# Kernel tuning notes

Hardware: AMD Instinct MI355X
Metric: run time of the kernel (lower is better)

The kernel has to match this reference:

```python
import jax, jax.numpy as jnp
import numpy as np

N = 8192
F_IN = 256
F_OUT = 128
SLOPE = 0.2
NEG_INF = -9000000000000000.0


def setup_inputs() -> dict:
    key = jax.random.key(0)
    k1, k2, k3, k4, k5 = jax.random.split(key, 5)
    x = jax.random.normal(k1, (N, F_IN), dtype=jnp.float32)
    adj = jax.random.randint(k2, (N, N), 0, 2).astype(jnp.float32)
    W = jax.random.normal(k3, (F_IN, F_OUT), dtype=jnp.float32) * (1.0 / np.sqrt(F_IN))
    a_src = jax.random.normal(k4, (F_OUT,), dtype=jnp.float32) * (1.0 / np.sqrt(F_OUT))
    a_dst = jax.random.normal(k5, (F_OUT,), dtype=jnp.float32) * (1.0 / np.sqrt(F_OUT))
    return {"x": x, "adj": adj, "W": W, "a_src": a_src, "a_dst": a_dst}


def reference(x, adj, W, a_src, a_dst):
    # h: (N, F_OUT)
    h = x @ W
    f_src = h @ a_src  # (N,)
    f_dst = h @ a_dst  # (N,)
    # additive attention scores: (N, N)
    e = f_src[:, None] + f_dst[None, :]
    e = jnp.where(e >= 0, e, SLOPE * e)  # leaky_relu
    e = jnp.where(adj > 0, e, NEG_INF)
    alpha = jax.nn.softmax(e, axis=1)  # (N, N)
    return alpha @ h  # (N, F_OUT)
```

## Files before the change

kernel.cpp:

```cpp
#include <hip/hip_runtime.h>
#include <hip/hip_bf16.h>

#define NN 8192
#define FIN 256
#define FO 128
#define ROWS 32
#define NCH 32
#define L2E 1.4426950408889634f
#define C2  0.28853900817779268f

typedef __bf16 bf16x8 __attribute__((ext_vector_type(8)));
typedef __bf16 bf16x2 __attribute__((ext_vector_type(2)));
typedef float  f32x4  __attribute__((ext_vector_type(4)));
typedef unsigned long long u64;
typedef u64 u64x2 __attribute__((ext_vector_type(2)));

__device__ __forceinline__ f32x4 ntload(const float* p) {
  return __builtin_nontemporal_load((const f32x4*)p);
}

__global__ __launch_bounds__(256) void k_proj(
    const float* __restrict__ x, const float* __restrict__ W,
    const float* __restrict__ a_src, const float* __restrict__ a_dst,
    __bf16* __restrict__ Bp, float* __restrict__ f_src, float* __restrict__ f_dst)
{
  __shared__ float xs[16 * FIN];
  __shared__ float fs[16], fd[16];
  const int tid = threadIdx.x;
  const int i0 = blockIdx.x * 16;

  const float4* xg = (const float4*)(x + (size_t)i0 * FIN);
  float4* xs4 = (float4*)xs;
  #pragma unroll
  for (int t = 0; t < 4; t++) xs4[tid + 256 * t] = xg[tid + 256 * t];
  if (tid < 16) { fs[tid] = 0.f; fd[tid] = 0.f; }
  __syncthreads();

  const int cq = tid & 31;
  const int rg = tid >> 5;
  const int c0 = cq * 4;
  const int r0 = rg * 2;
  float acc0[4] = {0.f,0.f,0.f,0.f};
  float acc1[4] = {0.f,0.f,0.f,0.f};
  const float* xr0 = xs + r0 * FIN;
  const float* xr1 = xs + (r0 + 1) * FIN;

  for (int k = 0; k < FIN; k += 4) {
    float4 xa = *(const float4*)(xr0 + k);
    float4 xb = *(const float4*)(xr1 + k);
    #pragma unroll
    for (int kk = 0; kk < 4; kk++) {
      float4 wv = *(const float4*)(W + (size_t)(k + kk) * FO + c0);
      float xav = ((const float*)&xa)[kk];
      float xbv = ((const float*)&xb)[kk];
      acc0[0] += xav * wv.x; acc0[1] += xav * wv.y;
      acc0[2] += xav * wv.z; acc0[3] += xav * wv.w;
      acc1[0] += xbv * wv.x; acc1[1] += xbv * wv.y;
      acc1[2] += xbv * wv.z; acc1[3] += xbv * wv.w;
    }
  }

  float4 as = *(const float4*)(a_src + c0);
  float4 ad = *(const float4*)(a_dst + c0);
  float ps0 = acc0[0]*as.x + acc0[1]*as.y + acc0[2]*as.z + acc0[3]*as.w;
  float ps1 = acc1[0]*as.x + acc1[1]*as.y + acc1[2]*as.z + acc1[3]*as.w;
  float pd0 = acc0[0]*ad.x + acc0[1]*ad.y + acc0[2]*ad.z + acc0[3]*ad.w;
  float pd1 = acc1[0]*ad.x + acc1[1]*ad.y + acc1[2]*ad.z + acc1[3]*ad.w;
  atomicAdd(&fs[r0],     ps0);
  atomicAdd(&fs[r0 + 1], ps1);
  atomicAdd(&fd[r0],     pd0);
  atomicAdd(&fd[r0 + 1], pd1);

  const int j0 = i0 + r0;
  const int kg = j0 >> 5;
  const int q  = (j0 >> 3) & 3;
  const int t0 = j0 & 7;
  #pragma unroll
  for (int c = 0; c < 4; c++) {
    const int n = c0 + c;
    bf16x2 v;
    v[0] = (__bf16)acc0[c];
    v[1] = (__bf16)acc1[c];
    size_t idx = ((size_t)(kg * 8 + (n >> 4)) * 64 + q * 16 + (n & 15)) * 8 + t0;
    *(bf16x2*)(Bp + idx) = v;
  }
  __syncthreads();
  if (tid < 16) { f_src[i0 + tid] = fs[tid]; f_dst[i0 + tid] = fd[tid]; }
}

__global__ __launch_bounds__(640) void k_attn(
    const float* __restrict__ adj, const __bf16* __restrict__ Bp,
    const float* __restrict__ f_src, const float* __restrict__ f_dst,
    float* __restrict__ out)
{
  __shared__ __align__(16) float G1[NN];
  __shared__ __align__(16) float G2[NN];
  __shared__ __align__(16) u64 msk[2][ROWS][5];
  __shared__ __align__(16) __bf16 af[2][2][8][64][8];
  __shared__ float lsum[ROWS];

  const int tid = threadIdx.x;
  const int w = tid >> 6;
  const int lane = tid & 63;
  const int i0 = blockIdx.x * ROWS;

  if (w >= 8) {
    const int pw = w - 8;
    const int prow0 = pw * 16;
    const float* abase = adj + (size_t)(i0 + prow0) * NN + lane * 4;

    f32x4 s0,s1,s2,s3,s4,s5,s6,s7,s8,s9,s10,s11,s12,s13,s14,s15;

#define PLOAD(c) {                                                            \
    const float* _b = abase + (size_t)(c) * 256;                              \
    s0=ntload(_b);        s1=ntload(_b+NN);       s2=ntload(_b+2*NN);         \
    s3=ntload(_b+3*NN);   s4=ntload(_b+4*NN);     s5=ntload(_b+5*NN);         \
    s6=ntload(_b+6*NN);   s7=ntload(_b+7*NN);     s8=ntload(_b+8*NN);         \
    s9=ntload(_b+9*NN);   s10=ntload(_b+10*NN);   s11=ntload(_b+11*NN);       \
    s12=ntload(_b+12*NN); s13=ntload(_b+13*NN);   s14=ntload(_b+14*NN);       \
    s15=ntload(_b+15*NN); }

#define PROW(sv, slot, r) {                                                   \
    u64 b0=__ballot(sv[0]>0.f), b1=__ballot(sv[1]>0.f);                       \
    u64 b2=__ballot(sv[2]>0.f), b3=__ballot(sv[3]>0.f);                       \
    if (lane < 4)                                                             \
      msk[slot][prow0 + (r)][lane] = lane==0?b0:lane==1?b1:lane==2?b2:b3; }

#define PPACK(slot) {                                                         \
    PROW(s0,slot,0)  PROW(s1,slot,1)  PROW(s2,slot,2)  PROW(s3,slot,3)        \
    PROW(s4,slot,4)  PROW(s5,slot,5)  PROW(s6,slot,6)  PROW(s7,slot,7)        \
    PROW(s8,slot,8)  PROW(s9,slot,9)  PROW(s10,slot,10) PROW(s11,slot,11)     \
    PROW(s12,slot,12) PROW(s13,slot,13) PROW(s14,slot,14) PROW(s15,slot,15) }

    PLOAD(0)
    PPACK(0)
    PLOAD(1)
    asm volatile("s_waitcnt lgkmcnt(0)" ::: "memory");
    __builtin_amdgcn_s_barrier();
    __builtin_amdgcn_sched_barrier(0);

    for (int k = 0; k < NCH; ++k) {
      if (k + 1 < NCH) {
        PPACK((k + 1) & 1)
        if (k + 2 < NCH) PLOAD(k + 2)
      }
      asm volatile("s_waitcnt lgkmcnt(0)" ::: "memory");
      __builtin_amdgcn_s_barrier();
      __builtin_amdgcn_sched_barrier(0);
    }
    __syncthreads();
#undef PLOAD
#undef PROW
#undef PPACK
  } else {
    const int m = lane & 15;
    const int q = lane >> 4;
    const int mt = w >> 2;
    const int ss = w & 3;
    const int nq = w & 3;

    #pragma unroll
    for (int t = 0; t < NN / 512; ++t) {
      int j = t * 512 + tid;
      float d = f_dst[j];
      G1[j] = __builtin_amdgcn_exp2f(d * L2E);
      G2[j] = __builtin_amdgcn_exp2f(d * C2);
    }
    if (tid < ROWS) lsum[tid] = 0.f;
    float s = f_src[i0 + mt * 16 + m];
    const float F1 = __builtin_amdgcn_exp2f(s * L2E);
    const float F2 = __builtin_amdgcn_exp2f(s * C2);

    f32x4 acc0 = (f32x4){0.f, 0.f, 0.f, 0.f};
    f32x4 acc1 = (f32x4){0.f, 0.f, 0.f, 0.f};
    float psum = 0.f;
    const int r0l = mt * 16 + m;

    __syncthreads();

    for (int c = 0; c < NCH; ++c) {
      const int cur = c & 1;

      {
        u64x2 Ma01 = *(const u64x2*)&msk[cur][r0l][0];
        u64x2 Ma23 = *(const u64x2*)&msk[cur][r0l][2];
        const u64 M0 = Ma01[0], M1 = Ma01[1], M2 = Ma23[0], M3 = Ma23[1];
        #pragma unroll
        for (int kg = 0; kg < 2; ++kg) {
          const int jj = c * 256 + ss * 64 + kg * 32 + q * 8;
          float4 u0 = *(const float4*)(G1 + jj);
          float4 u1 = *(const float4*)(G1 + jj + 4);
          float4 v0 = *(const float4*)(G2 + jj);
          float4 v1 = *(const float4*)(G2 + jj + 4);
          const unsigned b = ss * 16 + kg * 8 + q * 2;
          const unsigned e0 = (unsigned)(M0 >> b);
          const unsigned e1 = (unsigned)(M1 >> b);
          const unsigned e2 = (unsigned)(M2 >> b);
          const unsigned e3 = (unsigned)(M3 >> b);
          float p0 = (e0 & 1u) ? fmaxf(F1 * u0.x, F2 * v0.x) : 0.f;
          float p1 = (e1 & 1u) ? fmaxf(F1 * u0.y, F2 * v0.y) : 0.f;
          float p2 = (e2 & 1u) ? fmaxf(F1 * u0.z, F2 * v0.z) : 0.f;
          float p3 = (e3 & 1u) ? fmaxf(F1 * u0.w, F2 * v0.w) : 0.f;
          float p4 = (e0 & 2u) ? fmaxf(F1 * u1.x, F2 * v1.x) : 0.f;
          float p5 = (e1 & 2u) ? fmaxf(F1 * u1.y, F2 * v1.y) : 0.f;
          float p6 = (e2 & 2u) ? fmaxf(F1 * u1.z, F2 * v1.z) : 0.f;
          float p7 = (e3 & 2u) ? fmaxf(F1 * u1.w, F2 * v1.w) : 0.f;
          psum += ((p0 + p1) + (p2 + p3)) + ((p4 + p5) + (p6 + p7));
          bf16x8 a;
          a[0] = (__bf16)p0; a[1] = (__bf16)p1; a[2] = (__bf16)p2;
          a[3] = (__bf16)p3; a[4] = (__bf16)p4; a[5] = (__bf16)p5;
          a[6] = (__bf16)p6; a[7] = (__bf16)p7;
          *(bf16x8*)&af[cur][mt][ss * 2 + kg][lane][0] = a;
        }
      }
      __syncthreads();

      {
        const __bf16* bch = Bp + (size_t)c * 8 * 4096 + (size_t)(nq * 2) * 512 + lane * 8;
        const bf16x8* afp = (const bf16x8*)&af[cur][mt][0][lane][0];
        #pragma unroll
        for (int h = 0; h < 2; ++h) {
          bf16x8 b00 = *(const bf16x8*)(bch + (h * 4 + 0) * 4096);
          bf16x8 b10 = *(const bf16x8*)(bch + (h * 4 + 0) * 4096 + 512);
          bf16x8 b01 = *(const bf16x8*)(bch + (h * 4 + 1) * 4096);
          bf16x8 b11 = *(const bf16x8*)(bch + (h * 4 + 1) * 4096 + 512);
          bf16x8 b02 = *(const bf16x8*)(bch + (h * 4 + 2) * 4096);
          bf16x8 b12 = *(const bf16x8*)(bch + (h * 4 + 2) * 4096 + 512);
          bf16x8 b03 = *(const bf16x8*)(bch + (h * 4 + 3) * 4096);
          bf16x8 b13 = *(const bf16x8*)(bch + (h * 4 + 3) * 4096 + 512);
          bf16x8 a0 = afp[(h * 4 + 0) * 64];
          bf16x8 a1 = afp[(h * 4 + 1) * 64];
          bf16x8 a2 = afp[(h * 4 + 2) * 64];
          bf16x8 a3 = afp[(h * 4 + 3) * 64];
          acc0 = __builtin_amdgcn_mfma_f32_16x16x32_bf16(a0, b00, acc0, 0, 0, 0);
          acc1 = __builtin_amdgcn_mfma_f32_16x16x32_bf16(a0, b10, acc1, 0, 0, 0);
          acc0 = __builtin_amdgcn_mfma_f32_16x16x32_bf16(a1, b01, acc0, 0, 0, 0);
          acc1 = __builtin_amdgcn_mfma_f32_16x16x32_bf16(a1, b11, acc1, 0, 0, 0);
          acc0 = __builtin_amdgcn_mfma_f32_16x16x32_bf16(a2, b02, acc0, 0, 0, 0);
          acc1 = __builtin_amdgcn_mfma_f32_16x16x32_bf16(a2, b12, acc1, 0, 0, 0);
          acc0 = __builtin_amdgcn_mfma_f32_16x16x32_bf16(a3, b03, acc0, 0, 0, 0);
          acc1 = __builtin_amdgcn_mfma_f32_16x16x32_bf16(a3, b13, acc1, 0, 0, 0);
        }
      }
    }

    {
      float p = psum;
      p += __shfl_xor(p, 16);
      p += __shfl_xor(p, 32);
      if (lane < 16) atomicAdd(&lsum[mt * 16 + lane], p);
    }
    __syncthreads();

    const int rr0 = mt * 16 + q * 4;
    #pragma unroll
    for (int r = 0; r < 4; ++r) {
      const float inv = 1.0f / lsum[rr0 + r];
      float* orow = out + (size_t)(i0 + rr0 + r) * FO + (nq * 2) * 16 + m;
      orow[0]  = acc0[r] * inv;
      orow[16] = acc1[r] * inv;
    }
  }
}

extern "C" void kernel_launch(void* const* d_in, const int* in_sizes, int n_in,
                              void* d_out, int out_size, void* d_ws, size_t ws_size,
                              hipStream_t stream) {
  const float* x     = (const float*)d_in[0];
  const float* adj   = (const float*)d_in[1];
  const float* W     = (const float*)d_in[2];
  const float* a_src = (const float*)d_in[3];
  const float* a_dst = (const float*)d_in[4];
  float* out = (float*)d_out;

  char* ws = (char*)d_ws;
  __bf16* Bp   = (__bf16*)ws;
  float* f_src = (float*)(ws + 2097152);
  float* f_dst = (float*)(ws + 2097152 + 32768);

  hipLaunchKernelGGL(k_proj, dim3(512), dim3(256), 0, stream,
                     x, W, a_src, a_dst, Bp, f_src, f_dst);
  hipLaunchKernelGGL(k_attn, dim3(256), dim3(640), 0, stream,
                     adj, Bp, f_src, f_dst, out);
}
```

Before: 402.9 us.

## Move adjacency bitmask packing into the prep kernel across the whole GPU

Before, the attention kernel had two producer waves per block that streamed the fp32 adjacency and packed it into bitmasks in LDS alongside the compute waves. Now a separate set of 2048 blocks in the projection kernel packs all of adj into a global 8 MB bitmask buffer. The attention kernel reads its masks directly from global memory with a one-chunk register prefetch and runs with 512 threads. The goal is to spread the 256 MB adj read across all CUs, since the attention grid has only 256 blocks. The cost is an extra global write and read of the bitmask and a serialization point between the two kernels.

```diff
diff --git a/kernel.cpp b/kernel.cpp
--- a/kernel.cpp
+++ b/kernel.cpp
@@ -15,11 +15,8 @@
 typedef unsigned long long u64;
 typedef u64 u64x2 __attribute__((ext_vector_type(2)));
 
-__device__ __forceinline__ f32x4 ntload(const float* p) {
-  return __builtin_nontemporal_load((const f32x4*)p);
-}
-
-__global__ __launch_bounds__(256) void k_proj(
+__global__ __launch_bounds__(256) void k_prep(
+    const float* __restrict__ adj, u64* __restrict__ ab,
     const float* __restrict__ x, const float* __restrict__ W,
     const float* __restrict__ a_src, const float* __restrict__ a_dst,
     __bf16* __restrict__ Bp, float* __restrict__ f_src, float* __restrict__ f_dst)
@@ -27,7 +24,37 @@
   __shared__ float xs[16 * FIN];
   __shared__ float fs[16], fd[16];
   const int tid = threadIdx.x;
-  const int i0 = blockIdx.x * 16;
+
+  if (blockIdx.x < 2048) {
+    const int w = tid >> 6, lane = tid & 63;
+    const int row = blockIdx.x * 4 + w;
+    const float4* src = (const float4*)(adj + (size_t)row * NN) + lane;
+    u64* dst = ab + (size_t)row * 128;
+
+    for (int g = 0; g < 32; g += 2) {
+      float4 va = src[g * 64];
+      float4 vb = src[g * 64 + 64];
+      u64 a0 = __ballot(va.x > 0.f);
+      u64 a1 = __ballot(va.y > 0.f);
+      u64 a2 = __ballot(va.z > 0.f);
+      u64 a3 = __ballot(va.w > 0.f);
+      if (lane < 4) {
+        u64 mv = lane == 0 ? a0 : lane == 1 ? a1 : lane == 2 ? a2 : a3;
+        dst[g * 4 + lane] = mv;
+      }
+      u64 b0 = __ballot(vb.x > 0.f);
+      u64 b1 = __ballot(vb.y > 0.f);
+      u64 b2 = __ballot(vb.z > 0.f);
+      u64 b3 = __ballot(vb.w > 0.f);
+      if (lane < 4) {
+        u64 mv = lane == 0 ? b0 : lane == 1 ? b1 : lane == 2 ? b2 : b3;
+        dst[(g + 1) * 4 + lane] = mv;
+      }
+    }
+    return;
+  }
+
+  const int i0 = (blockIdx.x - 2048) * 16;
 
   const float4* xg = (const float4*)(x + (size_t)i0 * FIN);
   float4* xs4 = (float4*)xs;
@@ -88,178 +115,133 @@
   if (tid < 16) { f_src[i0 + tid] = fs[tid]; f_dst[i0 + tid] = fd[tid]; }
 }
 
-__global__ __launch_bounds__(640) void k_attn(
-    const float* __restrict__ adj, const __bf16* __restrict__ Bp,
+__global__ __launch_bounds__(512) void k_attn(
+    const u64* __restrict__ ab, const __bf16* __restrict__ Bp,
     const float* __restrict__ f_src, const float* __restrict__ f_dst,
     float* __restrict__ out)
 {
   __shared__ __align__(16) float G1[NN];
   __shared__ __align__(16) float G2[NN];
-  __shared__ __align__(16) u64 msk[2][ROWS][5];
   __shared__ __align__(16) __bf16 af[2][2][8][64][8];
   __shared__ float lsum[ROWS];
 
   const int tid = threadIdx.x;
   const int w = tid >> 6;
   const int lane = tid & 63;
+  const int m = lane & 15;
+  const int q = lane >> 4;
   const int i0 = blockIdx.x * ROWS;
-
-  if (w >= 8) {
-    const int pw = w - 8;
-    const int prow0 = pw * 16;
-    const float* abase = adj + (size_t)(i0 + prow0) * NN + lane * 4;
-
-    f32x4 s0,s1,s2,s3,s4,s5,s6,s7,s8,s9,s10,s11,s12,s13,s14,s15;
-
-#define PLOAD(c) {                                                            \
-    const float* _b = abase + (size_t)(c) * 256;                              \
-    s0=ntload(_b);        s1=ntload(_b+NN);       s2=ntload(_b+2*NN);         \
-    s3=ntload(_b+3*NN);   s4=ntload(_b+4*NN);     s5=ntload(_b+5*NN);         \
-    s6=ntload(_b+6*NN);   s7=ntload(_b+7*NN);     s8=ntload(_b+8*NN);         \
-    s9=ntload(_b+9*NN);   s10=ntload(_b+10*NN);   s11=ntload(_b+11*NN);       \
-    s12=ntload(_b+12*NN); s13=ntload(_b+13*NN);   s14=ntload(_b+14*NN);       \
-    s15=ntload(_b+15*NN); }
-
-#define PROW(sv, slot, r) {                                                   \
-    u64 b0=__ballot(sv[0]>0.f), b1=__ballot(sv[1]>0.f);                       \
-    u64 b2=__ballot(sv[2]>0.f), b3=__ballot(sv[3]>0.f);                       \
-    if (lane < 4)                                                             \
-      msk[slot][prow0 + (r)][lane] = lane==0?b0:lane==1?b1:lane==2?b2:b3; }
-
-#define PPACK(slot) {                                                         \
-    PROW(s0,slot,0)  PROW(s1,slot,1)  PROW(s2,slot,2)  PROW(s3,slot,3)        \
-    PROW(s4,slot,4)  PROW(s5,slot,5)  PROW(s6,slot,6)  PROW(s7,slot,7)        \
-    PROW(s8,slot,8)  PROW(s9,slot,9)  PROW(s10,slot,10) PROW(s11,slot,11)     \
-    PROW(s12,slot,12) PROW(s13,slot,13) PROW(s14,slot,14) PROW(s15,slot,15) }
-
-    PLOAD(0)
-    PPACK(0)
-    PLOAD(1)
-    asm volatile("s_waitcnt lgkmcnt(0)" ::: "memory");
-    __builtin_amdgcn_s_barrier();
-    __builtin_amdgcn_sched_barrier(0);
-
-    for (int k = 0; k < NCH; ++k) {
-      if (k + 1 < NCH) {
-        PPACK((k + 1) & 1)
-        if (k + 2 < NCH) PLOAD(k + 2)
-      }
-      asm volatile("s_waitcnt lgkmcnt(0)" ::: "memory");
-      __builtin_amdgcn_s_barrier();
-      __builtin_amdgcn_sched_barrier(0);
+  const int mt = w >> 2;
+  const int sq = w & 3;
+
+  const u64* mrow = ab + (size_t)(i0 + mt * 16 + m) * 128;
+  u64x2 Mlo = *(const u64x2*)(mrow);
+  u64x2 Mhi = *(const u64x2*)(mrow + 2);
+
+  #pragma unroll
+  for (int t = 0; t < NN / 512; ++t) {
+    int j = t * 512 + tid;
+    float d = f_dst[j];
+    G1[j] = __builtin_amdgcn_exp2f(d * L2E);
+    G2[j] = __builtin_amdgcn_exp2f(d * C2);
+  }
+  if (tid < ROWS) lsum[tid] = 0.f;
+  float s = f_src[i0 + mt * 16 + m];
+  const float F1 = __builtin_amdgcn_exp2f(s * L2E);
+  const float F2 = __builtin_amdgcn_exp2f(s * C2);
+
+  f32x4 acc0 = (f32x4){0.f, 0.f, 0.f, 0.f};
+  f32x4 acc1 = (f32x4){0.f, 0.f, 0.f, 0.f};
+  float psum = 0.f;
+
+  __syncthreads();
+
+  for (int c = 0; c < NCH; ++c) {
+    const int cur = c & 1;
+
+    const int cn = (c + 1 < NCH) ? c + 1 : c;
+    u64x2 Nlo = *(const u64x2*)(mrow + cn * 4);
+    u64x2 Nhi = *(const u64x2*)(mrow + cn * 4 + 2);
+
+    {
+      const u64 M0 = Mlo[0], M1 = Mlo[1], M2 = Mhi[0], M3 = Mhi[1];
+      #pragma unroll
+      for (int kg = 0; kg < 2; ++kg) {
+        const int jj = c * 256 + sq * 64 + kg * 32 + q * 8;
+        float4 u0 = *(const float4*)(G1 + jj);
+        float4 u1 = *(const float4*)(G1 + jj + 4);
+        float4 v0 = *(const float4*)(G2 + jj);
+        float4 v1 = *(const float4*)(G2 + jj + 4);
+        const unsigned b = sq * 16 + kg * 8 + q * 2;
+        const unsigned e0 = (unsigned)(M0 >> b);
+        const unsigned e1 = (unsigned)(M1 >> b);
+        const unsigned e2 = (unsigned)(M2 >> b);
+        const unsigned e3 = (unsigned)(M3 >> b);
+        float p0 = (e0 & 1u) ? fmaxf(F1 * u0.x, F2 * v0.x) : 0.f;
+        float p1 = (e1 & 1u) ? fmaxf(F1 * u0.y, F2 * v0.y) : 0.f;
+        float p2 = (e2 & 1u) ? fmaxf(F1 * u0.z, F2 * v0.z) : 0.f;
+        float p3 = (e3 & 1u) ? fmaxf(F1 * u0.w, F2 * v0.w) : 0.f;
+        float p4 = (e0 & 2u) ? fmaxf(F1 * u1.x, F2 * v1.x) : 0.f;
+        float p5 = (e1 & 2u) ? fmaxf(F1 * u1.y, F2 * v1.y) : 0.f;
+        float p6 = (e2 & 2u) ? fmaxf(F1 * u1.z, F2 * v1.z) : 0.f;
+        float p7 = (e3 & 2u) ? fmaxf(F1 * u1.w, F2 * v1.w) : 0.f;
+        psum += ((p0 + p1) + (p2 + p3)) + ((p4 + p5) + (p6 + p7));
+        bf16x8 a;
+        a[0] = (__bf16)p0; a[1] = (__bf16)p1; a[2] = (__bf16)p2;
+        a[3] = (__bf16)p3; a[4] = (__bf16)p4; a[5] = (__bf16)p5;
+        a[6] = (__bf16)p6; a[7] = (__bf16)p7;
+        *(bf16x8*)&af[cur][mt][sq * 2 + kg][lane][0] = a;
+      }
     }
     __syncthreads();
-#undef PLOAD
-#undef PROW
-#undef PPACK
-  } else {
-    const int m = lane & 15;
-    const int q = lane >> 4;
-    const int mt = w >> 2;
-    const int ss = w & 3;
-    const int nq = w & 3;
-
-    #pragma unroll
-    for (int t = 0; t < NN / 512; ++t) {
-      int j = t * 512 + tid;
-      float d = f_dst[j];
-      G1[j] = __builtin_amdgcn_exp2f(d * L2E);
-      G2[j] = __builtin_amdgcn_exp2f(d * C2);
-    }
-    if (tid < ROWS) lsum[tid] = 0.f;
-    float s = f_src[i0 + mt * 16 + m];
-    const float F1 = __builtin_amdgcn_exp2f(s * L2E);
-    const float F2 = __builtin_amdgcn_exp2f(s * C2);
-
-    f32x4 acc0 = (f32x4){0.f, 0.f, 0.f, 0.f};
-    f32x4 acc1 = (f32x4){0.f, 0.f, 0.f, 0.f};
-    float psum = 0.f;
-    const int r0l = mt * 16 + m;
-
-    __syncthreads();
-
-    for (int c = 0; c < NCH; ++c) {
-      const int cur = c & 1;
-
-      {
-        u64x2 Ma01 = *(const u64x2*)&msk[cur][r0l][0];
-        u64x2 Ma23 = *(const u64x2*)&msk[cur][r0l][2];
-        const u64 M0 = Ma01[0], M1 = Ma01[1], M2 = Ma23[0], M3 = Ma23[1];
-        #pragma unroll
-        for (int kg = 0; kg < 2; ++kg) {
-          const int jj = c * 256 + ss * 64 + kg * 32 + q * 8;
-          float4 u0 = *(const float4*)(G1 + jj);
-          float4 u1 = *(const float4*)(G1 + jj + 4);
-          float4 v0 = *(const float4*)(G2 + jj);
-          float4 v1 = *(const float4*)(G2 + jj + 4);
-          const unsigned b = ss * 16 + kg * 8 + q * 2;
-          const unsigned e0 = (unsigned)(M0 >> b);
-          const unsigned e1 = (unsigned)(M1 >> b);
-          const unsigned e2 = (unsigned)(M2 >> b);
-          const unsigned e3 = (unsigned)(M3 >> b);
-          float p0 = (e0 & 1u) ? fmaxf(F1 * u0.x, F2 * v0.x) : 0.f;
-          float p1 = (e1 & 1u) ? fmaxf(F1 * u0.y, F2 * v0.y) : 0.f;
-          float p2 = (e2 & 1u) ? fmaxf(F1 * u0.z, F2 * v0.z) : 0.f;
-          float p3 = (e3 & 1u) ? fmaxf(F1 * u0.w, F2 * v0.w) : 0.f;
-          float p4 = (e0 & 2u) ? fmaxf(F1 * u1.x, F2 * v1.x) : 0.f;
-          float p5 = (e1 & 2u) ? fmaxf(F1 * u1.y, F2 * v1.y) : 0.f;
-          float p6 = (e2 & 2u) ? fmaxf(F1 * u1.z, F2 * v1.z) : 0.f;
-          float p7 = (e3 & 2u) ? fmaxf(F1 * u1.w, F2 * v1.w) : 0.f;
-          psum += ((p0 + p1) + (p2 + p3)) + ((p4 + p5) + (p6 + p7));
-          bf16x8 a;
-          a[0] = (__bf16)p0; a[1] = (__bf16)p1; a[2] = (__bf16)p2;
-          a[3] = (__bf16)p3; a[4] = (__bf16)p4; a[5] = (__bf16)p5;
-          a[6] = (__bf16)p6; a[7] = (__bf16)p7;
-          *(bf16x8*)&af[cur][mt][ss * 2 + kg][lane][0] = a;
-        }
-      }
-      __syncthreads();
-
-      {
-        const __bf16* bch = Bp + (size_t)c * 8 * 4096 + (size_t)(nq * 2) * 512 + lane * 8;
-        const bf16x8* afp = (const bf16x8*)&af[cur][mt][0][lane][0];
-        #pragma unroll
-        for (int h = 0; h < 2; ++h) {
-          bf16x8 b00 = *(const bf16x8*)(bch + (h * 4 + 0) * 4096);
-          bf16x8 b10 = *(const bf16x8*)(bch + (h * 4 + 0) * 4096 + 512);
-          bf16x8 b01 = *(const bf16x8*)(bch + (h * 4 + 1) * 4096);
-          bf16x8 b11 = *(const bf16x8*)(bch + (h * 4 + 1) * 4096 + 512);
-          bf16x8 b02 = *(const bf16x8*)(bch + (h * 4 + 2) * 4096);
-          bf16x8 b12 = *(const bf16x8*)(bch + (h * 4 + 2) * 4096 + 512);
-          bf16x8 b03 = *(const bf16x8*)(bch + (h * 4 + 3) * 4096);
-          bf16x8 b13 = *(const bf16x8*)(bch + (h * 4 + 3) * 4096 + 512);
-          bf16x8 a0 = afp[(h * 4 + 0) * 64];
-          bf16x8 a1 = afp[(h * 4 + 1) * 64];
-          bf16x8 a2 = afp[(h * 4 + 2) * 64];
-          bf16x8 a3 = afp[(h * 4 + 3) * 64];
-          acc0 = __builtin_amdgcn_mfma_f32_16x16x32_bf16(a0, b00, acc0, 0, 0, 0);
-          acc1 = __builtin_amdgcn_mfma_f32_16x16x32_bf16(a0, b10, acc1, 0, 0, 0);
-          acc0 = __builtin_amdgcn_mfma_f32_16x16x32_bf16(a1, b01, acc0, 0, 0, 0);
-          acc1 = __builtin_amdgcn_mfma_f32_16x16x32_bf16(a1, b11, acc1, 0, 0, 0);
-          acc0 = __builtin_amdgcn_mfma_f32_16x16x32_bf16(a2, b02, acc0, 0, 0, 0);
-          acc1 = __builtin_amdgcn_mfma_f32_16x16x32_bf16(a2, b12, acc1, 0, 0, 0);
-          acc0 = __builtin_amdgcn_mfma_f32_16x16x32_bf16(a3, b03, acc0, 0, 0, 0);
-          acc1 = __builtin_amdgcn_mfma_f32_16x16x32_bf16(a3, b13, acc1, 0, 0, 0);
-        }
-      }
-    }
 
     {
-      float p = psum;
-      p += __shfl_xor(p, 16);
-      p += __shfl_xor(p, 32);
-      if (lane < 16) atomicAdd(&lsum[mt * 16 + lane], p);
-    }
-    __syncthreads();
-
-    const int rr0 = mt * 16 + q * 4;
-    #pragma unroll
-    for (int r = 0; r < 4; ++r) {
-      const float inv = 1.0f / lsum[rr0 + r];
-      float* orow = out + (size_t)(i0 + rr0 + r) * FO + (nq * 2) * 16 + m;
-      orow[0]  = acc0[r] * inv;
-      orow[16] = acc1[r] * inv;
-    }
+      const __bf16* bch = Bp + (size_t)c * 8 * 4096 + (size_t)(sq * 2) * 512 + lane * 8;
+      const bf16x8* afp = (const bf16x8*)&af[cur][mt][0][lane][0];
+      #pragma unroll
+      for (int h = 0; h < 2; ++h) {
+        bf16x8 b00 = *(const bf16x8*)(bch + (h * 4 + 0) * 4096);
+        bf16x8 b10 = *(const bf16x8*)(bch + (h * 4 + 0) * 4096 + 512);
+        bf16x8 b01 = *(const bf16x8*)(bch + (h * 4 + 1) * 4096);
+        bf16x8 b11 = *(const bf16x8*)(bch + (h * 4 + 1) * 4096 + 512);
+        bf16x8 b02 = *(const bf16x8*)(bch + (h * 4 + 2) * 4096);
+        bf16x8 b12 = *(const bf16x8*)(bch + (h * 4 + 2) * 4096 + 512);
+        bf16x8 b03 = *(const bf16x8*)(bch + (h * 4 + 3) * 4096);
+        bf16x8 b13 = *(const bf16x8*)(bch + (h * 4 + 3) * 4096 + 512);
+        bf16x8 a0 = afp[(h * 4 + 0) * 64];
+        bf16x8 a1 = afp[(h * 4 + 1) * 64];
+        bf16x8 a2 = afp[(h * 4 + 2) * 64];
+        bf16x8 a3 = afp[(h * 4 + 3) * 64];
+        acc0 = __builtin_amdgcn_mfma_f32_16x16x32_bf16(a0, b00, acc0, 0, 0, 0);
+        acc1 = __builtin_amdgcn_mfma_f32_16x16x32_bf16(a0, b10, acc1, 0, 0, 0);
+        acc0 = __builtin_amdgcn_mfma_f32_16x16x32_bf16(a1, b01, acc0, 0, 0, 0);
+        acc1 = __builtin_amdgcn_mfma_f32_16x16x32_bf16(a1, b11, acc1, 0, 0, 0);
+        acc0 = __builtin_amdgcn_mfma_f32_16x16x32_bf16(a2, b02, acc0, 0, 0, 0);
+        acc1 = __builtin_amdgcn_mfma_f32_16x16x32_bf16(a2, b12, acc1, 0, 0, 0);
+        acc0 = __builtin_amdgcn_mfma_f32_16x16x32_bf16(a3, b03, acc0, 0, 0, 0);
+        acc1 = __builtin_amdgcn_mfma_f32_16x16x32_bf16(a3, b13, acc1, 0, 0, 0);
+      }
+    }
+
+    Mlo = Nlo;
+    Mhi = Nhi;
+  }
+
+  {
+    float p = psum;
+    p += __shfl_xor(p, 16);
+    p += __shfl_xor(p, 32);
+    if (lane < 16) atomicAdd(&lsum[mt * 16 + lane], p);
+  }
+  __syncthreads();
+
+  const int rr0 = mt * 16 + q * 4;
+  #pragma unroll
+  for (int r = 0; r < 4; ++r) {
+    const float inv = 1.0f / lsum[rr0 + r];
+    float* orow = out + (size_t)(i0 + rr0 + r) * FO + (sq * 2) * 16 + m;
+    orow[0]  = acc0[r] * inv;
+    orow[16] = acc1[r] * inv;
   }
 }
 
@@ -277,9 +259,10 @@
   __bf16* Bp   = (__bf16*)ws;
   float* f_src = (float*)(ws + 2097152);
   float* f_dst = (float*)(ws + 2097152 + 32768);
-
-  hipLaunchKernelGGL(k_proj, dim3(512), dim3(256), 0, stream,
-                     x, W, a_src, a_dst, Bp, f_src, f_dst);
-  hipLaunchKernelGGL(k_attn, dim3(256), dim3(640), 0, stream,
-                     adj, Bp, f_src, f_dst, out);
+  u64*   ab    = (u64*)(ws + 4194304);
+
+  hipLaunchKernelGGL(k_prep, dim3(2560), dim3(256), 0, stream,
+                     adj, ab, x, W, a_src, a_dst, Bp, f_src, f_dst);
+  hipLaunchKernelGGL(k_attn, dim3(256), dim3(512), 0, stream,
+                     ab, Bp, f_src, f_dst, out);
 }
```

New measurement: 444.8 us. 1.1x slower.
